# Kernel tuning notes

Hardware: AMD Instinct MI355X
Metric: run time of the kernel (lower is better)

Reference implementation:

```python
import jax, jax.numpy as jnp
import numpy as np
import math

NUM_HEADS = 16
HEAD_SIZE = 64
SEQ_LEN = 2048
D_MODEL = NUM_HEADS * HEAD_SIZE
BATCH = 2


def _xavier(key, shape):
    fan_in, fan_out = shape[0], shape[1]
    limit = math.sqrt(6.0 / (fan_in + fan_out))
    return jax.random.uniform(key, shape, jnp.float32, -limit, limit)


def setup_inputs() -> dict:
    key = jax.random.key(0)
    ks = jax.random.split(key, 5)
    x = jax.random.normal(ks[0], (BATCH, SEQ_LEN, D_MODEL), jnp.float32)
    W_Q = _xavier(ks[1], (D_MODEL, D_MODEL))
    W_K = _xavier(ks[2], (D_MODEL, D_MODEL))
    W_V = _xavier(ks[3], (D_MODEL, D_MODEL))
    W_O = _xavier(ks[4], (D_MODEL, D_MODEL))
    zeros = jnp.zeros((D_MODEL,), jnp.float32)
    return {
        "x": x,
        "W_Q": W_Q, "W_K": W_K, "W_V": W_V, "W_O": W_O,
        "b_Q": zeros, "b_K": zeros, "b_V": zeros, "b_O": zeros,
    }


def _split_heads(t):
    # [B, S, H*d] -> [B, H, S, d]
    B, S, _ = t.shape
    return t.reshape(B, S, NUM_HEADS, HEAD_SIZE).transpose(0, 2, 1, 3)


def reference(x, W_Q, W_K, W_V, W_O, b_Q, b_K, b_V, b_O):
    q = _split_heads(x @ W_Q + b_Q)  # [B,H,S,d]
    k = _split_heads(x @ W_K + b_K)
    v = _split_heads(x @ W_V + b_V)

    # scores: [B,H,S,S]
    scores = jnp.einsum("bhqd,bhkd->bhqk", q, k)
    # Faithful to original: multiply by lower-triangular 0/1 mask, scale,
    # then add -10000 on strictly-upper positions (NOT -inf).
    tril = jnp.tril(jnp.ones((SEQ_LEN, SEQ_LEN), jnp.float32))
    neg_bias = jnp.triu(jnp.full((SEQ_LEN, SEQ_LEN), -10000.0, jnp.float32), 1)
    masked = scores * tril / np.sqrt(HEAD_SIZE).astype(np.float32) + neg_bias
    weights = jax.nn.softmax(masked, axis=-1)

    hs = jnp.einsum("bhqk,bhkd->bhqd", weights, v)  # [B,H,S,d]
    B = hs.shape[0]
    merged = hs.transpose(0, 2, 1, 3).reshape(B, SEQ_LEN, D_MODEL)
    return merged @ W_O + b_O
```

## Files before the change

### kernel.cpp

```cpp
#include <hip/hip_runtime.h>
#include <hip/hip_bf16.h>

#define S_LEN 2048
#define NH 16
#define HD 64
#define DM 1024
#define BATCH 2
#define M_ROWS (BATCH * S_LEN)
#define SCALE2 0.18033688011112043f

typedef float f32x4 __attribute__((ext_vector_type(4)));
typedef __bf16 bf16x8 __attribute__((ext_vector_type(8)));
typedef short short8 __attribute__((ext_vector_type(8)));

__device__ __forceinline__ unsigned short f2bf(float f) {
  unsigned u = __builtin_bit_cast(unsigned, f);
  u += 0x7FFFu + ((u >> 16) & 1u);
  return (unsigned short)(u >> 16);
}

__device__ __forceinline__ f32x4 mfma16(bf16x8 a, bf16x8 b, f32x4 c) {
  return __builtin_amdgcn_mfma_f32_16x16x32_bf16(a, b, c, 0, 0, 0);
}

__device__ __forceinline__ void gload_lds16(const void* g, void* l) {
  __builtin_amdgcn_global_load_lds(
      (const __attribute__((address_space(1))) void*)g,
      (__attribute__((address_space(3))) void*)l, 16, 0, 0);
}

__global__ __launch_bounds__(256) void cast_bf16_kernel(
    const float* __restrict__ in, unsigned short* __restrict__ out) {
  int i = blockIdx.x * 256 + threadIdx.x;
  const float4* p = (const float4*)in;
  float4 f0 = p[i * 2], f1 = p[i * 2 + 1];
  short8 o;
  o[0] = (short)f2bf(f0.x); o[1] = (short)f2bf(f0.y);
  o[2] = (short)f2bf(f0.z); o[3] = (short)f2bf(f0.w);
  o[4] = (short)f2bf(f1.x); o[5] = (short)f2bf(f1.y);
  o[6] = (short)f2bf(f1.z); o[7] = (short)f2bf(f1.w);
  ((short8*)out)[i] = o;
}

__global__ __launch_bounds__(256) void transpose_cast_kernel(
    const float* __restrict__ W0, const float* __restrict__ W1,
    const float* __restrict__ W2, const float* __restrict__ W3,
    unsigned short* __restrict__ out) {
  int z = blockIdx.z;
  const float* W = (z == 0) ? W0 : (z == 1) ? W1 : (z == 2) ? W2 : W3;
  __shared__ float tile[32][33];
  int tx = threadIdx.x & 31, ty = threadIdx.x >> 5;
  int bx = blockIdx.x * 32, by = blockIdx.y * 32;
#pragma unroll
  for (int i = 0; i < 4; ++i)
    tile[ty + i * 8][tx] = W[(size_t)(by + ty + i * 8) * DM + bx + tx];
  __syncthreads();
  unsigned short* o = out + (size_t)z * DM * DM;
#pragma unroll
  for (int i = 0; i < 4; ++i)
    o[(size_t)(bx + ty + i * 8) * DM + by + tx] = f2bf(tile[tx][ty + i * 8]);
}

template <int MODE>
__global__ __launch_bounds__(256) void gemm_bt_kernel(
    const unsigned short* __restrict__ A, const unsigned short* __restrict__ Bt,
    void* __restrict__ Cptr, const float* __restrict__ bias0,
    const float* __restrict__ bias1, const float* __restrict__ bias2,
    int M, int N, int K) {
  __shared__ __align__(16) unsigned short As[3][4096];
  __shared__ __align__(16) unsigned short Bs[3][4096];
  const int t = threadIdx.x, lane = t & 63;
  const int wid = t >> 6, wr = wid >> 1, wc = wid & 1;
  const int r16 = lane & 15, g = lane >> 4;
  const int m0 = blockIdx.y * 128, n0 = blockIdx.x * 128;
  const int nk = K >> 5;

  const int n1 = t, n2 = t + 256;
  const int r1g = t >> 2, c1g = (t & 3) * 8;
  const int r2g = (t + 256) >> 2;

  const unsigned short* ap1 = A + (size_t)(m0 + r1g) * K + c1g;
  const unsigned short* ap2 = A + (size_t)(m0 + r2g) * K + c1g;
  const unsigned short* bp1 = Bt + (size_t)(n0 + r1g) * K + c1g;
  const unsigned short* bp2 = Bt + (size_t)(n0 + r2g) * K + c1g;

#define GSTAGE(s)                          \
  gload_lds16(ap1, &As[s][n1 * 8]);        \
  gload_lds16(bp1, &Bs[s][n1 * 8]);        \
  gload_lds16(ap2, &As[s][n2 * 8]);        \
  gload_lds16(bp2, &Bs[s][n2 * 8]);        \
  ap1 += 32; ap2 += 32; bp1 += 32; bp2 += 32;

  f32x4 acc[4][4] = {};

  GSTAGE(0);
  GSTAGE(1);

  for (int kt = 0; kt < nk; ++kt) {
    const int cs = kt % 3;
    if (kt + 1 < nk) {
      asm volatile("s_waitcnt vmcnt(4)" ::: "memory");
    } else {
      asm volatile("s_waitcnt vmcnt(0)" ::: "memory");
    }
    __builtin_amdgcn_s_barrier();
    if (kt + 2 < nk) { GSTAGE((kt + 2) % 3); }

    bf16x8 af[4], bfr[4];
#pragma unroll
    for (int mi = 0; mi < 4; ++mi)
      af[mi] = *(const bf16x8*)&As[cs][(wr * 64 + mi * 16 + r16) * 32 + g * 8];
#pragma unroll
    for (int ni = 0; ni < 4; ++ni)
      bfr[ni] = *(const bf16x8*)&Bs[cs][(wc * 64 + ni * 16 + r16) * 32 + g * 8];
    __builtin_amdgcn_s_setprio(1);
#pragma unroll
    for (int mi = 0; mi < 4; ++mi)
#pragma unroll
      for (int ni = 0; ni < 4; ++ni)
        acc[mi][ni] = mfma16(af[mi], bfr[ni], acc[mi][ni]);
    __builtin_amdgcn_s_setprio(0);
  }
#undef GSTAGE

  if (MODE == 0) {
    unsigned short* Cb = (unsigned short*)Cptr;
#pragma unroll
    for (int ni = 0; ni < 4; ++ni) {
      int col = n0 + wc * 64 + ni * 16 + r16;
      int buf = col >> 10, cn = col & 1023;
      const float* bp = (buf == 0) ? bias0 : (buf == 1) ? bias1 : bias2;
      float bv = bp[cn];
      float sc = (buf == 0) ? SCALE2 : 1.0f;
#pragma unroll
      for (int mi = 0; mi < 4; ++mi) {
        int rowb = m0 + wr * 64 + mi * 16 + 4 * g;
#pragma unroll
        for (int j = 0; j < 4; ++j)
          Cb[(size_t)buf * 4194304u + (size_t)(rowb + j) * 1024 + cn] =
              __builtin_bit_cast(unsigned short, (__bf16)((acc[mi][ni][j] + bv) * sc));
      }
    }
  } else {
    float* Cf = (float*)Cptr;
#pragma unroll
    for (int ni = 0; ni < 4; ++ni) {
      int col = n0 + wc * 64 + ni * 16 + r16;
      float bv = bias0[col];
#pragma unroll
      for (int mi = 0; mi < 4; ++mi) {
        int rowb = m0 + wr * 64 + mi * 16 + 4 * g;
#pragma unroll
        for (int j = 0; j < 4; ++j)
          Cf[(size_t)(rowb + j) * N + col] = acc[mi][ni][j] + bv;
      }
    }
  }
}

__global__ __launch_bounds__(256) void vtrans_kernel(
    const unsigned short* __restrict__ V, unsigned short* __restrict__ Vt) {
  __shared__ __align__(16) unsigned short tile[128 * 72];
  const int t = threadIdx.x;
  const int s0 = blockIdx.x * 128;
  const int bh = blockIdx.y, b = bh >> 4, h = bh & 15;
#pragma unroll
  for (int p = 0; p < 4; ++p) {
    int idx = p * 256 + t;
    int sl = idx >> 3, c8 = (idx & 7) * 8;
    *(short8*)&tile[sl * 72 + c8] =
        *(const short8*)(V + (size_t)(b * S_LEN + s0 + sl) * DM + h * HD + c8);
  }
  __syncthreads();
#pragma unroll
  for (int p = 0; p < 4; ++p) {
    int idx = p * 256 + t;
    int dlow = idx & 7, sc = (idx >> 3) & 15, dh = idx >> 7;
    int d = dh * 8 + dlow, s8 = sc * 8;
    short8 o;
#pragma unroll
    for (int e = 0; e < 8; ++e) o[e] = (short)tile[(s8 + e) * 72 + d];
    *(short8*)(Vt + (size_t)(bh * HD + d) * S_LEN + s0 + s8) = o;
  }
}

#define M2FIX 8.0f

__global__ __launch_bounds__(256) void attn_kernel(
    const unsigned short* __restrict__ Qm, const unsigned short* __restrict__ Km,
    const unsigned short* __restrict__ VtG, unsigned short* __restrict__ Om) {
  const int t = threadIdx.x, lane = t & 63, w = t >> 6;
  const int r16 = lane & 15, g = lane >> 4;
  const int bid = blockIdx.x;
  const int xk = bid & 7, slot = bid >> 3;
  const int grp = xk + 8 * (slot >> 4);
  const int mq = slot & 15;
  const int h = grp & 15, b = grp >> 4;

  __shared__ __align__(16) unsigned short Ks[3][4096];
  __shared__ __align__(16) unsigned short Vs[3][4096];
  __shared__ __align__(16) unsigned short Pl[4608];

  const unsigned short* Kbase = Km + (size_t)(b * S_LEN) * DM + h * HD;
  const unsigned short* Vbase = VtG + (size_t)((b * NH + h) * HD) * S_LEN;

  const int n1 = t, n2 = t + 256;
  const int r1 = n1 >> 3, c1 = ((n1 & 7) ^ (r1 & 7)) * 8;
  const int r2 = n2 >> 3, c2 = ((n2 & 7) ^ (r2 & 7)) * 8;
  const int sx = r16 & 7;
  const int qloc = w * 16 + r16;

  unsigned short* Pw = &Pl[w * 1152];
  unsigned* Pw32 = (unsigned*)Pw;

#define STAGE(s)                          \
  gload_lds16(kp1, &Ks[s][n1 * 8]);       \
  gload_lds16(kp2, &Ks[s][n2 * 8]);       \
  gload_lds16(vp1, &Vs[s][n1 * 8]);       \
  gload_lds16(vp2, &Vs[s][n2 * 8]);       \
  kp1 += 64 * DM; kp2 += 64 * DM; vp1 += 64; vp2 += 64;

  for (int half = 0; half < 2; ++half) {
    const int qt = half ? 31 - mq : mq;
    const int q0 = qt * 64;
    const unsigned short* Qp = Qm + (size_t)(b * S_LEN + q0 + qloc) * DM + h * HD;
    bf16x8 qf0 = *(const bf16x8*)(Qp + g * 8);
    bf16x8 qf1 = *(const bf16x8*)(Qp + 32 + g * 8);

    f32x4 oacc[4] = {};
    float lsum = 0.f;
    const int ntk = qt + 1;

    const unsigned short* kp1 = Kbase + (size_t)r1 * DM + c1;
    const unsigned short* kp2 = Kbase + (size_t)r2 * DM + c2;
    const unsigned short* vp1 = Vbase + (size_t)r1 * S_LEN + c1;
    const unsigned short* vp2 = Vbase + (size_t)r2 * S_LEN + c2;

    __syncthreads();
    STAGE(0);
    STAGE(1);

    for (int kt = 0; kt < ntk; ++kt) {
      const int cs = kt % 3;
      if (kt + 1 < ntk) {
        asm volatile("s_waitcnt vmcnt(4)" ::: "memory");
      } else {
        asm volatile("s_waitcnt vmcnt(0)" ::: "memory");
      }
      __builtin_amdgcn_s_barrier();
      if (kt + 2 < ntk) { STAGE((kt + 2) % 3); }

      f32x4 st[4];
#pragma unroll
      for (int ni = 0; ni < 4; ++ni) {
        int row = ni * 16 + r16;
        f32x4 z = {};
        bf16x8 kf0 = *(const bf16x8*)&Ks[cs][row * 64 + ((g ^ sx) * 8)];
        bf16x8 kf1 = *(const bf16x8*)&Ks[cs][row * 64 + (((4 + g) ^ sx) * 8)];
        __builtin_amdgcn_s_setprio(1);
        st[ni] = mfma16(kf1, qf1, mfma16(kf0, qf0, z));
        __builtin_amdgcn_s_setprio(0);
      }

      float p[4][4];
#pragma unroll
      for (int ni = 0; ni < 4; ++ni)
#pragma unroll
        for (int j = 0; j < 4; ++j)
          p[ni][j] = __builtin_amdgcn_exp2f(st[ni][j] - M2FIX);
      if (kt == qt) {
#pragma unroll
        for (int ni = 0; ni < 4; ++ni)
#pragma unroll
          for (int j = 0; j < 4; ++j) {
            int kvl = ni * 16 + 4 * g + j;
            if (kvl > qloc) p[ni][j] = 0.f;
          }
      }
      lsum += ((p[0][0] + p[0][1]) + (p[0][2] + p[0][3])) +
              ((p[1][0] + p[1][1]) + (p[1][2] + p[1][3])) +
              ((p[2][0] + p[2][1]) + (p[2][2] + p[2][3])) +
              ((p[3][0] + p[3][1]) + (p[3][2] + p[3][3]));

#pragma unroll
      for (int ni = 0; ni < 4; ++ni) {
        union { __bf16 hh[4]; uint2 u; } cv;
        cv.hh[0] = (__bf16)p[ni][0];
        cv.hh[1] = (__bf16)p[ni][1];
        cv.hh[2] = (__bf16)p[ni][2];
        cv.hh[3] = (__bf16)p[ni][3];
        *(uint2*)&Pw32[r16 * 36 + ni * 8 + 2 * g] = cv.u;
      }
      bf16x8 pf0 = *(const bf16x8*)&Pw[r16 * 72 + g * 8];
      bf16x8 pf1 = *(const bf16x8*)&Pw[r16 * 72 + 32 + g * 8];

      __builtin_amdgcn_s_setprio(1);
#pragma unroll
      for (int di = 0; di < 4; ++di) {
        int row = di * 16 + r16;
        bf16x8 vf0 = *(const bf16x8*)&Vs[cs][row * 64 + ((g ^ sx) * 8)];
        bf16x8 vf1 = *(const bf16x8*)&Vs[cs][row * 64 + (((4 + g) ^ sx) * 8)];
        oacc[di] = mfma16(vf0, pf0, oacc[di]);
        oacc[di] = mfma16(vf1, pf1, oacc[di]);
      }
      __builtin_amdgcn_s_setprio(0);
    }

    lsum += __shfl_xor(lsum, 16);
    lsum += __shfl_xor(lsum, 32);
    float li = 1.0f / lsum;
    unsigned short* op = Om + (size_t)(b * S_LEN + q0 + qloc) * DM + h * HD;
#pragma unroll
    for (int di = 0; di < 4; ++di) {
      union { __bf16 hh[4]; uint2 u; } ov;
      ov.hh[0] = (__bf16)(oacc[di][0] * li);
      ov.hh[1] = (__bf16)(oacc[di][1] * li);
      ov.hh[2] = (__bf16)(oacc[di][2] * li);
      ov.hh[3] = (__bf16)(oacc[di][3] * li);
      *(uint2*)(op + di * 16 + 4 * g) = ov.u;
    }
  }
#undef STAGE
}

extern "C" void kernel_launch(void* const* d_in, const int* in_sizes, int n_in,
                              void* d_out, int out_size, void* d_ws, size_t ws_size,
                              hipStream_t stream) {
  (void)in_sizes; (void)n_in; (void)out_size; (void)ws_size;
  const float* x  = (const float*)d_in[0];
  const float* WQ = (const float*)d_in[1];
  const float* WK = (const float*)d_in[2];
  const float* WV = (const float*)d_in[3];
  const float* WO = (const float*)d_in[4];
  const float* bQ = (const float*)d_in[5];
  const float* bK = (const float*)d_in[6];
  const float* bV = (const float*)d_in[7];
  const float* bO = (const float*)d_in[8];

  char* ws = (char*)d_ws;
  unsigned short* xb  = (unsigned short*)(ws);
  unsigned short* wt  = (unsigned short*)(ws + (8u << 20));
  unsigned short* qb  = (unsigned short*)(ws + (16u << 20));
  unsigned short* hsb = (unsigned short*)(ws + (40u << 20));
  unsigned short* vt  = xb;

  cast_bf16_kernel<<<2048, 256, 0, stream>>>(x, xb);
  transpose_cast_kernel<<<dim3(32, 32, 4), 256, 0, stream>>>(WQ, WK, WV, WO, wt);
  gemm_bt_kernel<0><<<dim3(24, 32), 256, 0, stream>>>(
      xb, wt, (void*)qb, bQ, bK, bV, M_ROWS, 3072, DM);
  vtrans_kernel<<<dim3(16, 32), 256, 0, stream>>>(qb + 8388608u, vt);
  attn_kernel<<<512, 256, 0, stream>>>(qb, qb + 4194304u, vt, hsb);
  gemm_bt_kernel<1><<<dim3(8, 32), 256, 0, stream>>>(
      hsb, wt + 3u * 1048576u, d_out, bO, nullptr, nullptr, M_ROWS, DM, DM);
}
```

Baseline: 120.7 us.

## Fuse V transpose into QKV GEMM epilogue and widen attention blocks to 128 queries

```diff
diff --git a/kernel.cpp b/kernel.cpp
--- a/kernel.cpp
+++ b/kernel.cpp
@@ -8,6 +8,7 @@
 #define BATCH 2
 #define M_ROWS (BATCH * S_LEN)
 #define SCALE2 0.18033688011112043f
+#define M2FIX 8.0f
 
 typedef float f32x4 __attribute__((ext_vector_type(4)));
 typedef __bf16 bf16x8 __attribute__((ext_vector_type(8)));
@@ -125,20 +126,38 @@
 
   if (MODE == 0) {
     unsigned short* Cb = (unsigned short*)Cptr;
-#pragma unroll
-    for (int ni = 0; ni < 4; ++ni) {
-      int col = n0 + wc * 64 + ni * 16 + r16;
-      int buf = col >> 10, cn = col & 1023;
-      const float* bp = (buf == 0) ? bias0 : (buf == 1) ? bias1 : bias2;
-      float bv = bp[cn];
-      float sc = (buf == 0) ? SCALE2 : 1.0f;
-#pragma unroll
-      for (int mi = 0; mi < 4; ++mi) {
-        int rowb = m0 + wr * 64 + mi * 16 + 4 * g;
-#pragma unroll
-        for (int j = 0; j < 4; ++j)
-          Cb[(size_t)buf * 4194304u + (size_t)(rowb + j) * 1024 + cn] =
-              __builtin_bit_cast(unsigned short, (__bf16)((acc[mi][ni][j] + bv) * sc));
+    const int buf = n0 >> 10;
+    if (buf < 2) {
+      const float* bp = buf ? bias1 : bias0;
+      const float sc = buf ? 1.0f : SCALE2;
+#pragma unroll
+      for (int ni = 0; ni < 4; ++ni) {
+        int cn = (n0 & 1023) + wc * 64 + ni * 16 + r16;
+        float bv = bp[cn];
+#pragma unroll
+        for (int mi = 0; mi < 4; ++mi) {
+          int rowb = m0 + wr * 64 + mi * 16 + 4 * g;
+#pragma unroll
+          for (int j = 0; j < 4; ++j)
+            Cb[(size_t)buf * 4194304u + (size_t)(rowb + j) * 1024 + cn] =
+                __builtin_bit_cast(unsigned short, (__bf16)((acc[mi][ni][j] + bv) * sc));
+        }
+      }
+    } else {
+#pragma unroll
+      for (int ni = 0; ni < 4; ++ni) {
+        int cn = (n0 & 1023) + wc * 64 + ni * 16 + r16;
+        float bv = bias2[cn];
+        int hh = cn >> 6, d = cn & 63;
+#pragma unroll
+        for (int mi = 0; mi < 4; ++mi) {
+          int rowb = m0 + wr * 64 + mi * 16 + 4 * g;
+          int bb = rowb >> 11, s = rowb & 2047;
+          union { __bf16 hh4[4]; uint2 u; } cv;
+#pragma unroll
+          for (int j = 0; j < 4; ++j) cv.hh4[j] = (__bf16)(acc[mi][ni][j] + bv);
+          *(uint2*)&Cb[8388608u + (((size_t)((bb * 16 + hh) * 64 + d)) << 11) + s] = cv.u;
+        }
       }
     }
   } else {
@@ -158,97 +177,64 @@
   }
 }
 
-__global__ __launch_bounds__(256) void vtrans_kernel(
-    const unsigned short* __restrict__ V, unsigned short* __restrict__ Vt) {
-  __shared__ __align__(16) unsigned short tile[128 * 72];
-  const int t = threadIdx.x;
-  const int s0 = blockIdx.x * 128;
-  const int bh = blockIdx.y, b = bh >> 4, h = bh & 15;
-#pragma unroll
-  for (int p = 0; p < 4; ++p) {
-    int idx = p * 256 + t;
-    int sl = idx >> 3, c8 = (idx & 7) * 8;
-    *(short8*)&tile[sl * 72 + c8] =
-        *(const short8*)(V + (size_t)(b * S_LEN + s0 + sl) * DM + h * HD + c8);
-  }
-  __syncthreads();
-#pragma unroll
-  for (int p = 0; p < 4; ++p) {
-    int idx = p * 256 + t;
-    int dlow = idx & 7, sc = (idx >> 3) & 15, dh = idx >> 7;
-    int d = dh * 8 + dlow, s8 = sc * 8;
-    short8 o;
-#pragma unroll
-    for (int e = 0; e < 8; ++e) o[e] = (short)tile[(s8 + e) * 72 + d];
-    *(short8*)(Vt + (size_t)(bh * HD + d) * S_LEN + s0 + s8) = o;
-  }
-}
-
-#define M2FIX 8.0f
-
-__global__ __launch_bounds__(256) void attn_kernel(
+__global__ __launch_bounds__(512, 4) void attn_kernel(
     const unsigned short* __restrict__ Qm, const unsigned short* __restrict__ Km,
     const unsigned short* __restrict__ VtG, unsigned short* __restrict__ Om) {
   const int t = threadIdx.x, lane = t & 63, w = t >> 6;
   const int r16 = lane & 15, g = lane >> 4;
   const int bid = blockIdx.x;
-  const int xk = bid & 7, slot = bid >> 3;
-  const int grp = xk + 8 * (slot >> 4);
-  const int mq = slot & 15;
+  const int xcd = bid & 7, slot = bid >> 3;
+  const int u = slot & 7;
+  const int grp = xcd * 4 + (slot >> 3);
   const int h = grp & 15, b = grp >> 4;
 
   __shared__ __align__(16) unsigned short Ks[3][4096];
   __shared__ __align__(16) unsigned short Vs[3][4096];
-  __shared__ __align__(16) unsigned short Pl[4608];
+  __shared__ __align__(16) unsigned short Pl[8 * 1152];
 
   const unsigned short* Kbase = Km + (size_t)(b * S_LEN) * DM + h * HD;
   const unsigned short* Vbase = VtG + (size_t)((b * NH + h) * HD) * S_LEN;
 
-  const int n1 = t, n2 = t + 256;
-  const int r1 = n1 >> 3, c1 = ((n1 & 7) ^ (r1 & 7)) * 8;
-  const int r2 = n2 >> 3, c2 = ((n2 & 7) ^ (r2 & 7)) * 8;
+  const int rk = t >> 3, ck = ((t & 7) ^ (rk & 7)) * 8;
   const int sx = r16 & 7;
   const int qloc = w * 16 + r16;
 
   unsigned short* Pw = &Pl[w * 1152];
   unsigned* Pw32 = (unsigned*)Pw;
 
-#define STAGE(s)                          \
-  gload_lds16(kp1, &Ks[s][n1 * 8]);       \
-  gload_lds16(kp2, &Ks[s][n2 * 8]);       \
-  gload_lds16(vp1, &Vs[s][n1 * 8]);       \
-  gload_lds16(vp2, &Vs[s][n2 * 8]);       \
-  kp1 += 64 * DM; kp2 += 64 * DM; vp1 += 64; vp2 += 64;
+#define STAGE(s, kv0)                                                   \
+  gload_lds16(Kbase + (size_t)((kv0) + rk) * DM + ck, &Ks[s][t * 8]);   \
+  gload_lds16(Vbase + (size_t)rk * S_LEN + (kv0) + ck, &Vs[s][t * 8]);
 
   for (int half = 0; half < 2; ++half) {
-    const int qt = half ? 31 - mq : mq;
-    const int q0 = qt * 64;
-    const unsigned short* Qp = Qm + (size_t)(b * S_LEN + q0 + qloc) * DM + h * HD;
+    const int su = half ? 15 - u : u;
+    const int qb0 = su * 128;
+    const int qg = qb0 + qloc;
+    const int wqmin = qb0 + w * 16;
+    const unsigned short* Qp = Qm + (size_t)(b * S_LEN + qg) * DM + h * HD;
     bf16x8 qf0 = *(const bf16x8*)(Qp + g * 8);
     bf16x8 qf1 = *(const bf16x8*)(Qp + 32 + g * 8);
 
     f32x4 oacc[4] = {};
     float lsum = 0.f;
-    const int ntk = qt + 1;
-
-    const unsigned short* kp1 = Kbase + (size_t)r1 * DM + c1;
-    const unsigned short* kp2 = Kbase + (size_t)r2 * DM + c2;
-    const unsigned short* vp1 = Vbase + (size_t)r1 * S_LEN + c1;
-    const unsigned short* vp2 = Vbase + (size_t)r2 * S_LEN + c2;
+    const int ntk = 2 * su + 2;
 
     __syncthreads();
-    STAGE(0);
-    STAGE(1);
+    STAGE(0, 0);
+    STAGE(1, 64);
 
     for (int kt = 0; kt < ntk; ++kt) {
       const int cs = kt % 3;
       if (kt + 1 < ntk) {
-        asm volatile("s_waitcnt vmcnt(4)" ::: "memory");
+        asm volatile("s_waitcnt vmcnt(2)" ::: "memory");
       } else {
         asm volatile("s_waitcnt vmcnt(0)" ::: "memory");
       }
       __builtin_amdgcn_s_barrier();
-      if (kt + 2 < ntk) { STAGE((kt + 2) % 3); }
+      if (kt + 2 < ntk) { STAGE((kt + 2) % 3, (kt + 2) * 64); }
+
+      const int kv0 = kt * 64;
+      if (kv0 > wqmin + 15) continue;
 
       f32x4 st[4];
 #pragma unroll
@@ -268,13 +254,13 @@
 #pragma unroll
         for (int j = 0; j < 4; ++j)
           p[ni][j] = __builtin_amdgcn_exp2f(st[ni][j] - M2FIX);
-      if (kt == qt) {
+      if (kv0 + 63 > wqmin) {
 #pragma unroll
         for (int ni = 0; ni < 4; ++ni)
 #pragma unroll
           for (int j = 0; j < 4; ++j) {
-            int kvl = ni * 16 + 4 * g + j;
-            if (kvl > qloc) p[ni][j] = 0.f;
+            int kvg = kv0 + ni * 16 + 4 * g + j;
+            if (kvg > qg) p[ni][j] = 0.f;
           }
       }
       lsum += ((p[0][0] + p[0][1]) + (p[0][2] + p[0][3])) +
@@ -309,7 +295,7 @@
     lsum += __shfl_xor(lsum, 16);
     lsum += __shfl_xor(lsum, 32);
     float li = 1.0f / lsum;
-    unsigned short* op = Om + (size_t)(b * S_LEN + q0 + qloc) * DM + h * HD;
+    unsigned short* op = Om + (size_t)(b * S_LEN + qg) * DM + h * HD;
 #pragma unroll
     for (int di = 0; di < 4; ++di) {
       union { __bf16 hh[4]; uint2 u; } ov;
@@ -342,14 +328,12 @@
   unsigned short* wt  = (unsigned short*)(ws + (8u << 20));
   unsigned short* qb  = (unsigned short*)(ws + (16u << 20));
   unsigned short* hsb = (unsigned short*)(ws + (40u << 20));
-  unsigned short* vt  = xb;
 
   cast_bf16_kernel<<<2048, 256, 0, stream>>>(x, xb);
   transpose_cast_kernel<<<dim3(32, 32, 4), 256, 0, stream>>>(WQ, WK, WV, WO, wt);
   gemm_bt_kernel<0><<<dim3(24, 32), 256, 0, stream>>>(
       xb, wt, (void*)qb, bQ, bK, bV, M_ROWS, 3072, DM);
-  vtrans_kernel<<<dim3(16, 32), 256, 0, stream>>>(qb + 8388608u, vt);
-  attn_kernel<<<512, 256, 0, stream>>>(qb, qb + 4194304u, vt, hsb);
+  attn_kernel<<<256, 512, 0, stream>>>(qb, qb + 4194304u, qb + 8388608u, hsb);
   gemm_bt_kernel<1><<<dim3(8, 32), 256, 0, stream>>>(
       hsb, wt + 3u * 1048576u, d_out, bO, nullptr, nullptr, M_ROWS, DM, DM);
 }
```

Measured after the change: 127.2 us. 5.4% more time.
